# Kernel tuning notes

Measured on AMD Instinct MI355X. Metric: run time of the kernel, lower is better.

## Reference

```python
import jax, jax.numpy as jnp
import numpy as np

N = 50000
E = 800000
IN_DIM = 128
HID = 32
OUT_DIM = 64
HEADS = 4
NEG_SLOPE = 0.2  # DGL GATConv default leaky_relu slope


def setup_inputs() -> dict:
    key = jax.random.key(0)
    ks = jax.random.split(key, 16)
    h = jax.random.normal(ks[0], (N, IN_DIM), dtype=jnp.float32)
    src = jax.random.randint(ks[1], (E,), 0, N, dtype=jnp.int32)
    dst = jax.random.randint(ks[2], (E,), 0, N, dtype=jnp.int32)
    s = 0.05
    # layer 1: in 128 -> heads*32 = 128
    W1 = jax.random.normal(ks[3], (IN_DIM, HEADS * HID), dtype=jnp.float32) * s
    al1 = jax.random.normal(ks[4], (HEADS, HID), dtype=jnp.float32) * s
    ar1 = jax.random.normal(ks[5], (HEADS, HID), dtype=jnp.float32) * s
    # layer 2: in 128 -> heads*32 = 128
    W2 = jax.random.normal(ks[6], (HEADS * HID, HEADS * HID), dtype=jnp.float32) * s
    al2 = jax.random.normal(ks[7], (HEADS, HID), dtype=jnp.float32) * s
    ar2 = jax.random.normal(ks[8], (HEADS, HID), dtype=jnp.float32) * s
    # last layer: in 128 -> heads*64 = 256 (needs residual projection)
    W3 = jax.random.normal(ks[9], (HEADS * HID, HEADS * OUT_DIM), dtype=jnp.float32) * s
    al3 = jax.random.normal(ks[10], (HEADS, OUT_DIM), dtype=jnp.float32) * s
    ar3 = jax.random.normal(ks[11], (HEADS, OUT_DIM), dtype=jnp.float32) * s
    resW3 = jax.random.normal(ks[12], (HEADS * HID, HEADS * OUT_DIM), dtype=jnp.float32) * s
    return {"h": h, "W1": W1, "al1": al1, "ar1": ar1, "W2": W2, "al2": al2,
            "ar2": ar2, "W3": W3, "al3": al3, "ar3": ar3, "resW3": resW3,
            "src": src, "dst": dst}


def gat_layer(h, src, dst, W, al, ar, heads, out_feats, res_W=None, act=None):
    n = h.shape[0]
    feat = (h @ W).reshape(n, heads, out_feats)          # [N,H,D]
    el = jnp.einsum('nhd,hd->nh', feat, al)               # [N,H]
    er = jnp.einsum('nhd,hd->nh', feat, ar)               # [N,H]
    e = jax.nn.leaky_relu(el[src] + er[dst], NEG_SLOPE)   # [E,H]
    m = jax.ops.segment_max(e, dst, num_segments=n)       # per-dst max, [N,H]
    ex = jnp.exp(e - m[dst])
    denom = jax.ops.segment_sum(ex, dst, num_segments=n)  # [N,H]
    alpha = ex / denom[dst]                               # edge softmax, [E,H]
    msg = feat[src] * alpha[:, :, None]                   # [E,H,D]
    rst = jax.ops.segment_sum(msg, dst, num_segments=n)   # [N,H,D]
    res = (h @ res_W) if res_W is not None else h
    rst = rst + res.reshape(n, heads, out_feats)
    if act is not None:
        rst = act(rst)
    return rst


def reference(h, W1, al1, ar1, W2, al2, ar2, W3, al3, ar3, resW3, src, dst):
    n = h.shape[0]
    x = gat_layer(h, src, dst, W1, al1, ar1, HEADS, HID, act=jax.nn.relu)
    x = x.reshape(n, -1)
    # feat_drop=0.3 on layer 2 omitted (eval/deterministic mode)
    x = gat_layer(x, src, dst, W2, al2, ar2, HEADS, HID, act=jax.nn.relu)
    x = x.reshape(n, -1)
    x = gat_layer(x, src, dst, W3, al3, ar3, HEADS, OUT_DIM, res_W=resW3)
    return x.mean(axis=1)  # mean over heads -> [N, OUT_DIM]
```

## Files before the change

kernel.cpp:

```cpp
#include <hip/hip_runtime.h>
#include <hip/hip_bf16.h>
#include <math.h>


#define NEG_SLOPE 0.2f

typedef __attribute__((ext_vector_type(8))) __bf16 bf16x8;
typedef __attribute__((ext_vector_type(4))) float f32x4;

__device__ __forceinline__ float leaky(float x) { return fmaxf(x, NEG_SLOPE * x); }
__device__ __forceinline__ ushort f2bf(float f) {
    unsigned u = __float_as_uint(f);
    return (ushort)((u + 0x7fffu + ((u >> 16) & 1u)) >> 16);
}
__device__ __forceinline__ float bf2f(ushort b) { return __uint_as_float(((unsigned)b) << 16); }
__device__ __forceinline__ float lo16f(unsigned v) { return __uint_as_float(v << 16); }
__device__ __forceinline__ float hi16f(unsigned v) { return __uint_as_float(v & 0xffff0000u); }


__global__ void hist_kernel(const int* __restrict__ dst, int* __restrict__ deg, int E) {
    int i = blockIdx.x * blockDim.x + threadIdx.x;
    if (i < E) atomicAdd(&deg[dst[i]], 1);
}

__global__ void block_scan_kernel(const int* __restrict__ deg, int* __restrict__ loc,
                                  int* __restrict__ bsum, int n) {
    __shared__ int sm[1024];
    const int tid = threadIdx.x;
    const int i = blockIdx.x * 1024 + tid;
    int v = (i < n) ? deg[i] : 0;
    sm[tid] = v;
    __syncthreads();
    for (int off = 1; off < 1024; off <<= 1) {
        int t = (tid >= off) ? sm[tid - off] : 0;
        __syncthreads();
        sm[tid] += t;
        __syncthreads();
    }
    if (i < n) loc[i] = sm[tid] - v;
    if (tid == 1023) bsum[blockIdx.x] = sm[1023];
}

__global__ void scan_bsum_kernel(int* __restrict__ bsum, int nb, int* __restrict__ total_out) {
    const int lane = threadIdx.x;
    int v = (lane < nb) ? bsum[lane] : 0;
    int orig = v;
    for (int off = 1; off < 64; off <<= 1) {
        int t = __shfl_up(v, off);
        if (lane >= off) v += t;
    }
    if (lane < nb) bsum[lane] = v - orig;
    if (lane == 63) *total_out = v;
}

__global__ void apply_scan_kernel(const int* __restrict__ loc, const int* __restrict__ bsum,
                                  int* __restrict__ row_ptr, int* __restrict__ cursor, int n) {
    int i = blockIdx.x * blockDim.x + threadIdx.x;
    if (i < n) {
        int v = loc[i] + bsum[i >> 10];
        row_ptr[i] = v;
        cursor[i]  = v;
    }
}

__global__ void scatter_kernel(const int* __restrict__ src, const int* __restrict__ dst,
                               int* __restrict__ cursor, int* __restrict__ ssrc, int E) {
    int i = blockIdx.x * blockDim.x + threadIdx.x;
    if (i < E) {
        int s = src[i];
        int pos = atomicAdd(&cursor[dst[i]], 1);
        ssrc[pos] = s;
    }
}


__global__ void cast_split_kernel(const float* __restrict__ in, ushort* __restrict__ hi,
                                  ushort* __restrict__ lo, int n4) {
    int i = blockIdx.x * blockDim.x + threadIdx.x;
    if (i >= n4) return;
    float4 v = ((const float4*)in)[i];
    ushort4 h, l;
    h.x = f2bf(v.x); l.x = f2bf(v.x - bf2f(h.x));
    h.y = f2bf(v.y); l.y = f2bf(v.y - bf2f(h.y));
    h.z = f2bf(v.z); l.z = f2bf(v.z - bf2f(h.z));
    h.w = f2bf(v.w); l.w = f2bf(v.w - bf2f(h.w));
    ((ushort4*)hi)[i] = h;
    ((ushort4*)lo)[i] = l;
}

__global__ void castT_kernel(const float* __restrict__ in, ushort* __restrict__ hi, int Ncols) {
    int i = blockIdx.x * blockDim.x + threadIdx.x;
    if (i >= 128 * Ncols) return;
    int c = i >> 7, k = i & 127;
    float v = in[k * Ncols + c];
    int kd = k ^ ((c & 7) << 3);
    hi[c * 128 + kd] = f2bf(v);
}

__global__ void fold_resW_kernel(const float* __restrict__ rW3, ushort* __restrict__ hi) {
    int i = blockIdx.x * blockDim.x + threadIdx.x;
    if (i >= 64 * 128) return;
    int c = i >> 7, k = i & 127;
    const float* row = rW3 + (size_t)k * 256;
    float v = 0.25f * ((row[c] + row[64 + c]) + (row[128 + c] + row[192 + c]));
    int kd = k ^ ((c & 7) << 3);
    hi[c * 128 + kd] = f2bf(v);
}


__global__ void __launch_bounds__(256)
gemm_kernel(const ushort* __restrict__ Ah, const ushort* __restrict__ Bth,
            ushort* __restrict__ Cb, float* __restrict__ Cf,
            const float* __restrict__ alv, const float* __restrict__ arv,
            float* __restrict__ el, float* __restrict__ er,
            int M, int Ncols, int dshift) {
    __shared__ ushort Ws[64 * 128];
    const int tid = threadIdx.x;
    const int wv = tid >> 6;
    const int lane = tid & 63;
    const int l15 = lane & 15;
    const int g = lane >> 4;
    const int bm = blockIdx.x * 128 + wv * 32;
    const int bn = blockIdx.y * 64;

    {
        const uint4* gh = (const uint4*)(Bth + (size_t)bn * 128);
        uint4* sh = (uint4*)Ws;
#pragma unroll
        for (int it = 0; it < 4; ++it) {
            sh[it * 256 + tid] = gh[it * 256 + tid];
        }
    }
    __syncthreads();

    const int m0 = bm + l15;
    const int m1 = bm + 16 + l15;
    const int mc0 = (m0 < M) ? m0 : (M - 1);
    const int mc1 = (m1 < M) ? m1 : (M - 1);
    bf16x8 xh[2][4];
#pragma unroll
    for (int kk = 0; kk < 4; ++kk) {
        xh[0][kk] = *(const bf16x8*)(Ah + (size_t)mc0 * 128 + kk * 32 + g * 8);
        xh[1][kk] = *(const bf16x8*)(Ah + (size_t)mc1 * 128 + kk * 32 + g * 8);
    }

    f32x4 acc[2][4] = {};
    const int swz = (l15 & 7) << 4;
#pragma unroll
    for (int n = 0; n < 4; ++n) {
        const int colb = (n * 16 + l15) * 256;
#pragma unroll
        for (int kk = 0; kk < 4; ++kk) {
            const int boff = colb + ((kk * 64 + g * 16) ^ swz);
            bf16x8 wh = *(const bf16x8*)((const char*)Ws + boff);
            acc[0][n] = __builtin_amdgcn_mfma_f32_16x16x32_bf16(wh, xh[0][kk], acc[0][n], 0, 0, 0);
            acc[1][n] = __builtin_amdgcn_mfma_f32_16x16x32_bf16(wh, xh[1][kk], acc[1][n], 0, 0, 0);
        }
    }

#pragma unroll
    for (int mf = 0; mf < 2; ++mf) {
        const int m = (mf == 0) ? m0 : m1;
        const bool valid = (m < M);
        if (valid) {
            size_t ro = (size_t)m * Ncols;
#pragma unroll
            for (int n = 0; n < 4; ++n) {
                int col = bn + n * 16 + g * 4;
                if (Cb) {
                    ushort4 o;
                    o.x = f2bf(acc[mf][n][0]); o.y = f2bf(acc[mf][n][1]);
                    o.z = f2bf(acc[mf][n][2]); o.w = f2bf(acc[mf][n][3]);
                    *(ushort4*)&Cb[ro + col] = o;
                }
                if (Cf) {
                    *(float4*)&Cf[ro + col] = make_float4(acc[mf][n][0], acc[mf][n][1],
                                                          acc[mf][n][2], acc[mf][n][3]);
                }
            }
        }
        if (alv) {
            float e0 = 0.f, e1 = 0.f, r0 = 0.f, r1 = 0.f;
#pragma unroll
            for (int n = 0; n < 4; ++n) {
#pragma unroll
                for (int r = 0; r < 4; ++r) {
                    int col = n * 16 + g * 4 + r;
                    float c = acc[mf][n][r];
                    float av = alv[bn + col];
                    float bv = arv[bn + col];
                    if ((col >> dshift) == 0) { e0 += c * av; r0 += c * bv; }
                    else                      { e1 += c * av; r1 += c * bv; }
                }
            }
            e0 += __shfl_xor(e0, 16); e0 += __shfl_xor(e0, 32);
            e1 += __shfl_xor(e1, 16); e1 += __shfl_xor(e1, 32);
            r0 += __shfl_xor(r0, 16); r0 += __shfl_xor(r0, 32);
            r1 += __shfl_xor(r1, 16); r1 += __shfl_xor(r1, 32);
            if (valid && g == 0) {
                int h0 = bn >> dshift;
                el[m * 4 + h0] = e0;
                er[m * 4 + h0] = r0;
                if (dshift == 5) {
                    el[m * 4 + h0 + 1] = e1;
                    er[m * 4 + h0 + 1] = r1;
                }
            }
        }
    }
}


__global__ void __launch_bounds__(256)
aggregate12_kernel(const ushort* __restrict__ featb, const float* __restrict__ el,
                   const float* __restrict__ er, const int* __restrict__ row_ptr,
                   const int* __restrict__ ssrc, ushort* __restrict__ xbh,
                   ushort* __restrict__ xbl, int n) {
    const int wid = threadIdx.x >> 6;
    const int lane = threadIdx.x & 63;
    const int node = blockIdx.x * 4 + wid;
    if (node >= n) return;
    const int beg = row_ptr[node];
    const int end = row_ptr[node + 1];
    const int hh = lane >> 4;
    const float erh = er[node * 4 + hh];

    float ssum = 0.f, a0 = 0.f, a1 = 0.f;
    int p = beg;
    for (; p + 8 <= end; p += 8) {
        int s[8];
        float e[8];
        unsigned v[8];
#pragma unroll
        for (int j = 0; j < 8; ++j) s[j] = __builtin_amdgcn_readfirstlane(ssrc[p + j]);
#pragma unroll
        for (int j = 0; j < 8; ++j) v[j] = *(const unsigned*)&featb[(size_t)s[j] * 128 + lane * 2];
#pragma unroll
        for (int j = 0; j < 8; ++j) e[j] = el[s[j] * 4 + hh];
#pragma unroll
        for (int j = 0; j < 8; ++j) {
            float w0 = __expf(leaky(e[j] + erh));
            ssum += w0;
            a0 += w0 * lo16f(v[j]);
            a1 += w0 * hi16f(v[j]);
        }
    }
    for (; p < end; ++p) {
        int s = __builtin_amdgcn_readfirstlane(ssrc[p]);
        float w0 = __expf(leaky(el[s * 4 + hh] + erh));
        unsigned v = *(const unsigned*)&featb[(size_t)s * 128 + lane * 2];
        ssum += w0;
        a0 += w0 * lo16f(v);
        a1 += w0 * hi16f(v);
    }
    float inv = (end > beg) ? 1.f / ssum : 0.f;
    size_t o = (size_t)node * 128 + lane * 2;
    unsigned rh = *(const unsigned*)&xbh[o];
    unsigned rl = *(const unsigned*)&xbl[o];
    float r0 = fmaxf(a0 * inv + lo16f(rh) + lo16f(rl), 0.f);
    float r1 = fmaxf(a1 * inv + hi16f(rh) + hi16f(rl), 0.f);
    ushort h0 = f2bf(r0), h1 = f2bf(r1);
    ushort l0 = f2bf(r0 - bf2f(h0)), l1 = f2bf(r1 - bf2f(h1));
    *(unsigned*)&xbh[o] = (unsigned)h0 | ((unsigned)h1 << 16);
    *(unsigned*)&xbl[o] = (unsigned)l0 | ((unsigned)l1 << 16);
}


__global__ void __launch_bounds__(256)
aggregate3_kernel(const ushort* __restrict__ featb, const float* __restrict__ el,
                  const float* __restrict__ er, const int* __restrict__ row_ptr,
                  const int* __restrict__ ssrc, const float* __restrict__ resmean,
                  float* __restrict__ out, int n) {
    const int wid = threadIdx.x >> 6;
    const int lane = threadIdx.x & 63;
    const int node = blockIdx.x * 4 + wid;
    if (node >= n) return;
    const int beg = row_ptr[node];
    const int end = row_ptr[node + 1];
    const int hh = lane >> 4;
    const int dd = (lane & 15) * 4;
    const int off = hh * 64 + dd;
    const float erh = er[node * 4 + hh];

    float c0 = 0.f, c1 = 0.f, c2 = 0.f, c3 = 0.f, ssum = 0.f;
    int p = beg;
    for (; p + 8 <= end; p += 8) {
        int s[8];
        float e[8];
        uint2 v[8];
#pragma unroll
        for (int j = 0; j < 8; ++j) s[j] = __builtin_amdgcn_readfirstlane(ssrc[p + j]);
#pragma unroll
        for (int j = 0; j < 8; ++j) v[j] = *(const uint2*)&featb[(size_t)s[j] * 256 + off];
#pragma unroll
        for (int j = 0; j < 8; ++j) e[j] = el[s[j] * 4 + hh];
#pragma unroll
        for (int j = 0; j < 8; ++j) {
            float w0 = __expf(leaky(e[j] + erh));
            ssum += w0;
            c0 += w0 * lo16f(v[j].x);
            c1 += w0 * hi16f(v[j].x);
            c2 += w0 * lo16f(v[j].y);
            c3 += w0 * hi16f(v[j].y);
        }
    }
    for (; p < end; ++p) {
        int s = __builtin_amdgcn_readfirstlane(ssrc[p]);
        float w0 = __expf(leaky(el[s * 4 + hh] + erh));
        uint2 v = *(const uint2*)&featb[(size_t)s * 256 + off];
        ssum += w0;
        c0 += w0 * lo16f(v.x);
        c1 += w0 * hi16f(v.x);
        c2 += w0 * lo16f(v.y);
        c3 += w0 * hi16f(v.y);
    }
    float inv = (end > beg) ? 1.f / ssum : 0.f;
    float r0 = c0 * inv, r1 = c1 * inv, r2 = c2 * inv, r3 = c3 * inv;
    r0 += __shfl_xor(r0, 16); r0 += __shfl_xor(r0, 32);
    r1 += __shfl_xor(r1, 16); r1 += __shfl_xor(r1, 32);
    r2 += __shfl_xor(r2, 16); r2 += __shfl_xor(r2, 32);
    r3 += __shfl_xor(r3, 16); r3 += __shfl_xor(r3, 32);
    if (hh == 0) {
        float4 rm = *(const float4*)&resmean[(size_t)node * 64 + dd];
        *(float4*)&out[(size_t)node * 64 + dd] =
            make_float4(0.25f * r0 + rm.x, 0.25f * r1 + rm.y,
                        0.25f * r2 + rm.z, 0.25f * r3 + rm.w);
    }
}


extern "C" void kernel_launch(void* const* d_in, const int* in_sizes, int n_in,
                              void* d_out, int out_size, void* d_ws, size_t ws_size,
                              hipStream_t stream) {
    const float* h   = (const float*)d_in[0];
    const float* W1  = (const float*)d_in[1];
    const float* al1 = (const float*)d_in[2];
    const float* ar1 = (const float*)d_in[3];
    const float* W2  = (const float*)d_in[4];
    const float* al2 = (const float*)d_in[5];
    const float* ar2 = (const float*)d_in[6];
    const float* W3  = (const float*)d_in[7];
    const float* al3 = (const float*)d_in[8];
    const float* ar3 = (const float*)d_in[9];
    const float* rW3 = (const float*)d_in[10];
    const int* src   = (const int*)d_in[11];
    const int* dstv  = (const int*)d_in[12];
    const int N = in_sizes[0] / 128;
    const int E = in_sizes[11];
    float* out = (float*)d_out;

    char* p = (char*)d_ws;
    auto alloc = [&](size_t bytes) -> char* {
        char* q = p;
        p += (bytes + 255) & ~(size_t)255;
        return q;
    };
    int*    row_ptr = (int*)alloc((size_t)(N + 1) * 4);
    int*    cursor  = (int*)alloc((size_t)N * 4);
    int*    loc     = (int*)alloc((size_t)N * 4);
    int*    bsum    = (int*)alloc(64 * 4);
    int*    ssrc    = (int*)alloc((size_t)E * 4);
    float*  el      = (float*)alloc((size_t)N * 16);
    float*  er      = (float*)alloc((size_t)N * 16);
    ushort* featb   = (ushort*)alloc((size_t)N * 256 * 2);
    ushort* xbh     = (ushort*)alloc((size_t)N * 128 * 2);
    ushort* xbl     = (ushort*)alloc((size_t)N * 128 * 2);
    ushort* W1th = (ushort*)alloc(128 * 128 * 2);
    ushort* W2th = (ushort*)alloc(128 * 128 * 2);
    ushort* W3th = (ushort*)alloc(256 * 128 * 2);
    ushort* rWmh = (ushort*)alloc(64 * 128 * 2);
    float*  resmean = (float*)alloc((size_t)N * 64 * 4);

    hipMemsetAsync(cursor, 0, (size_t)N * 4, stream);
    hist_kernel<<<(E + 255) / 256, 256, 0, stream>>>(dstv, cursor, E);
    int nb = (N + 1023) / 1024;
    block_scan_kernel<<<nb, 1024, 0, stream>>>(cursor, loc, bsum, N);
    scan_bsum_kernel<<<1, 64, 0, stream>>>(bsum, nb, row_ptr + N);
    apply_scan_kernel<<<(N + 255) / 256, 256, 0, stream>>>(loc, bsum, row_ptr, cursor, N);
    scatter_kernel<<<(E + 255) / 256, 256, 0, stream>>>(src, dstv, cursor, ssrc, E);

    cast_split_kernel<<<(N * 128 / 4 + 255) / 256, 256, 0, stream>>>(h, xbh, xbl, N * 128 / 4);
    castT_kernel<<<(128 * 128 + 255) / 256, 256, 0, stream>>>(W1, W1th, 128);
    castT_kernel<<<(128 * 128 + 255) / 256, 256, 0, stream>>>(W2, W2th, 128);
    castT_kernel<<<(128 * 256 + 255) / 256, 256, 0, stream>>>(W3, W3th, 256);
    fold_resW_kernel<<<(64 * 128 + 255) / 256, 256, 0, stream>>>(rW3, rWmh);

    const int gx = (N + 127) / 128;
    dim3 g1(gx, 2);
    dim3 g3(gx, 4);
    dim3 gr(gx, 1);
    int agg_grid = (N + 3) / 4;

    gemm_kernel<<<g1, 256, 0, stream>>>(xbh, W1th, featb, nullptr,
                                        al1, ar1, el, er, N, 128, 5);
    aggregate12_kernel<<<agg_grid, 256, 0, stream>>>(featb, el, er, row_ptr, ssrc, xbh, xbl, N);

    gemm_kernel<<<g1, 256, 0, stream>>>(xbh, W2th, featb, nullptr,
                                        al2, ar2, el, er, N, 128, 5);
    aggregate12_kernel<<<agg_grid, 256, 0, stream>>>(featb, el, er, row_ptr, ssrc, xbh, xbl, N);

    gemm_kernel<<<g3, 256, 0, stream>>>(xbh, W3th, featb, nullptr,
                                        al3, ar3, el, er, N, 256, 6);
    gemm_kernel<<<gr, 256, 0, stream>>>(xbh, rWmh, nullptr, resmean,
                                        nullptr, nullptr, nullptr, nullptr, N, 64, 6);
    aggregate3_kernel<<<agg_grid, 256, 0, stream>>>(featb, el, er, row_ptr, ssrc, resmean, out, N);
}
```

Measured before the change: 418.3 us.

## Fuse prep casts into one kernel, merge residual GEMM into layer-3 GEMM

Five small cast/transpose kernels become one prep kernel, which now writes only the bf16 high part of h. Layer 1's residual is read as fp32 straight from h in the aggregate kernel, so the lo buffer is no longer written there. The separate residual-projection GEMM is folded into the layer-3 GEMM: blocks with blockIdx.y==0 also load the folded residual weights into LDS and compute a second accumulator. This saves launches and a second read of xbh, but makes y==0 blocks do more work and doubles dynamic LDS for all blocks of that launch, which may lower occupancy.

After: 401.7 us. 1.04x faster.

```diff
diff --git a/kernel.cpp b/kernel.cpp
--- a/kernel.cpp
+++ b/kernel.cpp
@@ -74,47 +74,55 @@
 }
 
 
-__global__ void cast_split_kernel(const float* __restrict__ in, ushort* __restrict__ hi,
-                                  ushort* __restrict__ lo, int n4) {
+__global__ void prep_kernel(const float* __restrict__ h, ushort* __restrict__ xbh,
+                            const float* __restrict__ W1, ushort* __restrict__ W1th,
+                            const float* __restrict__ W2, ushort* __restrict__ W2th,
+                            const float* __restrict__ W3, ushort* __restrict__ W3th,
+                            const float* __restrict__ rW3, ushort* __restrict__ rWmh,
+                            int nh4) {
     int i = blockIdx.x * blockDim.x + threadIdx.x;
-    if (i >= n4) return;
-    float4 v = ((const float4*)in)[i];
-    ushort4 h, l;
-    h.x = f2bf(v.x); l.x = f2bf(v.x - bf2f(h.x));
-    h.y = f2bf(v.y); l.y = f2bf(v.y - bf2f(h.y));
-    h.z = f2bf(v.z); l.z = f2bf(v.z - bf2f(h.z));
-    h.w = f2bf(v.w); l.w = f2bf(v.w - bf2f(h.w));
-    ((ushort4*)hi)[i] = h;
-    ((ushort4*)lo)[i] = l;
-}
-
-__global__ void castT_kernel(const float* __restrict__ in, ushort* __restrict__ hi, int Ncols) {
-    int i = blockIdx.x * blockDim.x + threadIdx.x;
-    if (i >= 128 * Ncols) return;
-    int c = i >> 7, k = i & 127;
-    float v = in[k * Ncols + c];
-    int kd = k ^ ((c & 7) << 3);
-    hi[c * 128 + kd] = f2bf(v);
-}
-
-__global__ void fold_resW_kernel(const float* __restrict__ rW3, ushort* __restrict__ hi) {
-    int i = blockIdx.x * blockDim.x + threadIdx.x;
-    if (i >= 64 * 128) return;
-    int c = i >> 7, k = i & 127;
-    const float* row = rW3 + (size_t)k * 256;
-    float v = 0.25f * ((row[c] + row[64 + c]) + (row[128 + c] + row[192 + c]));
-    int kd = k ^ ((c & 7) << 3);
-    hi[c * 128 + kd] = f2bf(v);
+    if (i < nh4) {
+        float4 v = ((const float4*)h)[i];
+        ushort4 o;
+        o.x = f2bf(v.x); o.y = f2bf(v.y); o.z = f2bf(v.z); o.w = f2bf(v.w);
+        ((ushort4*)xbh)[i] = o;
+        return;
+    }
+    int j = i - nh4;
+    if (j < 16384) {
+        int c = j >> 7, k = j & 127;
+        int kd = k ^ ((c & 7) << 3);
+        W1th[c * 128 + kd] = f2bf(W1[k * 128 + c]);
+    } else if (j < 32768) {
+        j -= 16384;
+        int c = j >> 7, k = j & 127;
+        int kd = k ^ ((c & 7) << 3);
+        W2th[c * 128 + kd] = f2bf(W2[k * 128 + c]);
+    } else if (j < 65536) {
+        j -= 32768;
+        int c = j >> 7, k = j & 127;
+        int kd = k ^ ((c & 7) << 3);
+        W3th[c * 128 + kd] = f2bf(W3[k * 256 + c]);
+    } else if (j < 73728) {
+        j -= 65536;
+        int c = j >> 7, k = j & 127;
+        const float* row = rW3 + (size_t)k * 256;
+        float v = 0.25f * ((row[c] + row[64 + c]) + (row[128 + c] + row[192 + c]));
+        int kd = k ^ ((c & 7) << 3);
+        rWmh[c * 128 + kd] = f2bf(v);
+    }
 }
 
 
 __global__ void __launch_bounds__(256)
 gemm_kernel(const ushort* __restrict__ Ah, const ushort* __restrict__ Bth,
-            ushort* __restrict__ Cb, float* __restrict__ Cf,
+            const ushort* __restrict__ B2th,
+            ushort* __restrict__ Cb, float* __restrict__ C2f,
             const float* __restrict__ alv, const float* __restrict__ arv,
             float* __restrict__ el, float* __restrict__ er,
             int M, int Ncols, int dshift) {
-    __shared__ ushort Ws[64 * 128];
+    extern __shared__ ushort Ws[];
+    ushort* Ws2 = Ws + 64 * 128;
     const int tid = threadIdx.x;
     const int wv = tid >> 6;
     const int lane = tid & 63;
@@ -122,13 +130,18 @@
     const int g = lane >> 4;
     const int bm = blockIdx.x * 128 + wv * 32;
     const int bn = blockIdx.y * 64;
+    const bool do2 = (B2th != nullptr) && (blockIdx.y == 0);
 
     {
         const uint4* gh = (const uint4*)(Bth + (size_t)bn * 128);
         uint4* sh = (uint4*)Ws;
 #pragma unroll
-        for (int it = 0; it < 4; ++it) {
-            sh[it * 256 + tid] = gh[it * 256 + tid];
+        for (int it = 0; it < 4; ++it) sh[it * 256 + tid] = gh[it * 256 + tid];
+        if (do2) {
+            const uint4* g2 = (const uint4*)B2th;
+            uint4* s2 = (uint4*)Ws2;
+#pragma unroll
+            for (int it = 0; it < 4; ++it) s2[it * 256 + tid] = g2[it * 256 + tid];
         }
     }
     __syncthreads();
@@ -145,6 +158,7 @@
     }
 
     f32x4 acc[2][4] = {};
+    f32x4 acc2[2][4] = {};
     const int swz = (l15 & 7) << 4;
 #pragma unroll
     for (int n = 0; n < 4; ++n) {
@@ -155,6 +169,11 @@
             bf16x8 wh = *(const bf16x8*)((const char*)Ws + boff);
             acc[0][n] = __builtin_amdgcn_mfma_f32_16x16x32_bf16(wh, xh[0][kk], acc[0][n], 0, 0, 0);
             acc[1][n] = __builtin_amdgcn_mfma_f32_16x16x32_bf16(wh, xh[1][kk], acc[1][n], 0, 0, 0);
+            if (do2) {
+                bf16x8 w2 = *(const bf16x8*)((const char*)Ws2 + boff);
+                acc2[0][n] = __builtin_amdgcn_mfma_f32_16x16x32_bf16(w2, xh[0][kk], acc2[0][n], 0, 0, 0);
+                acc2[1][n] = __builtin_amdgcn_mfma_f32_16x16x32_bf16(w2, xh[1][kk], acc2[1][n], 0, 0, 0);
+            }
         }
     }
 
@@ -167,15 +186,14 @@
 #pragma unroll
             for (int n = 0; n < 4; ++n) {
                 int col = bn + n * 16 + g * 4;
-                if (Cb) {
-                    ushort4 o;
-                    o.x = f2bf(acc[mf][n][0]); o.y = f2bf(acc[mf][n][1]);
-                    o.z = f2bf(acc[mf][n][2]); o.w = f2bf(acc[mf][n][3]);
-                    *(ushort4*)&Cb[ro + col] = o;
-                }
-                if (Cf) {
-                    *(float4*)&Cf[ro + col] = make_float4(acc[mf][n][0], acc[mf][n][1],
-                                                          acc[mf][n][2], acc[mf][n][3]);
+                ushort4 o;
+                o.x = f2bf(acc[mf][n][0]); o.y = f2bf(acc[mf][n][1]);
+                o.z = f2bf(acc[mf][n][2]); o.w = f2bf(acc[mf][n][3]);
+                *(ushort4*)&Cb[ro + col] = o;
+                if (do2) {
+                    *(float4*)&C2f[(size_t)m * 64 + n * 16 + g * 4] =
+                        make_float4(acc2[mf][n][0], acc2[mf][n][1],
+                                    acc2[mf][n][2], acc2[mf][n][3]);
                 }
             }
         }
@@ -214,8 +232,9 @@
 __global__ void __launch_bounds__(256)
 aggregate12_kernel(const ushort* __restrict__ featb, const float* __restrict__ el,
                    const float* __restrict__ er, const int* __restrict__ row_ptr,
-                   const int* __restrict__ ssrc, ushort* __restrict__ xbh,
-                   ushort* __restrict__ xbl, int n) {
+                   const int* __restrict__ ssrc, const float* __restrict__ resf,
+                   const ushort* __restrict__ rxh, const ushort* __restrict__ rxl,
+                   ushort* __restrict__ xbh, ushort* __restrict__ xbl, int n) {
     const int wid = threadIdx.x >> 6;
     const int lane = threadIdx.x & 63;
     const int node = blockIdx.x * 4 + wid;
@@ -255,10 +274,18 @@
     }
     float inv = (end > beg) ? 1.f / ssum : 0.f;
     size_t o = (size_t)node * 128 + lane * 2;
-    unsigned rh = *(const unsigned*)&xbh[o];
-    unsigned rl = *(const unsigned*)&xbl[o];
-    float r0 = fmaxf(a0 * inv + lo16f(rh) + lo16f(rl), 0.f);
-    float r1 = fmaxf(a1 * inv + hi16f(rh) + hi16f(rl), 0.f);
+    float rb0, rb1;
+    if (resf) {
+        float2 f = *(const float2*)&resf[o];
+        rb0 = f.x; rb1 = f.y;
+    } else {
+        unsigned rh = *(const unsigned*)&rxh[o];
+        unsigned rl = *(const unsigned*)&rxl[o];
+        rb0 = lo16f(rh) + lo16f(rl);
+        rb1 = hi16f(rh) + hi16f(rl);
+    }
+    float r0 = fmaxf(a0 * inv + rb0, 0.f);
+    float r1 = fmaxf(a1 * inv + rb1, 0.f);
     ushort h0 = f2bf(r0), h1 = f2bf(r1);
     ushort l0 = f2bf(r0 - bf2f(h0)), l1 = f2bf(r1 - bf2f(h1));
     *(unsigned*)&xbh[o] = (unsigned)h0 | ((unsigned)h1 << 16);
@@ -379,29 +406,28 @@
     apply_scan_kernel<<<(N + 255) / 256, 256, 0, stream>>>(loc, bsum, row_ptr, cursor, N);
     scatter_kernel<<<(E + 255) / 256, 256, 0, stream>>>(src, dstv, cursor, ssrc, E);
 
-    cast_split_kernel<<<(N * 128 / 4 + 255) / 256, 256, 0, stream>>>(h, xbh, xbl, N * 128 / 4);
-    castT_kernel<<<(128 * 128 + 255) / 256, 256, 0, stream>>>(W1, W1th, 128);
-    castT_kernel<<<(128 * 128 + 255) / 256, 256, 0, stream>>>(W2, W2th, 128);
-    castT_kernel<<<(128 * 256 + 255) / 256, 256, 0, stream>>>(W3, W3th, 256);
-    fold_resW_kernel<<<(64 * 128 + 255) / 256, 256, 0, stream>>>(rW3, rWmh);
+    const int nh4 = N * 32;
+    prep_kernel<<<(nh4 + 73728 + 255) / 256, 256, 0, stream>>>(
+        h, xbh, W1, W1th, W2, W2th, W3, W3th, rW3, rWmh, nh4);
 
     const int gx = (N + 127) / 128;
     dim3 g1(gx, 2);
     dim3 g3(gx, 4);
-    dim3 gr(gx, 1);
     int agg_grid = (N + 3) / 4;
-
-    gemm_kernel<<<g1, 256, 0, stream>>>(xbh, W1th, featb, nullptr,
-                                        al1, ar1, el, er, N, 128, 5);
-    aggregate12_kernel<<<agg_grid, 256, 0, stream>>>(featb, el, er, row_ptr, ssrc, xbh, xbl, N);
-
-    gemm_kernel<<<g1, 256, 0, stream>>>(xbh, W2th, featb, nullptr,
-                                        al2, ar2, el, er, N, 128, 5);
-    aggregate12_kernel<<<agg_grid, 256, 0, stream>>>(featb, el, er, row_ptr, ssrc, xbh, xbl, N);
-
-    gemm_kernel<<<g3, 256, 0, stream>>>(xbh, W3th, featb, nullptr,
-                                        al3, ar3, el, er, N, 256, 6);
-    gemm_kernel<<<gr, 256, 0, stream>>>(xbh, rWmh, nullptr, resmean,
-                                        nullptr, nullptr, nullptr, nullptr, N, 64, 6);
+    const size_t lds1 = 64 * 128 * sizeof(ushort);
+    const size_t lds2 = 2 * 64 * 128 * sizeof(ushort);
+
+    gemm_kernel<<<g1, 256, lds1, stream>>>(xbh, W1th, nullptr, featb, nullptr,
+                                           al1, ar1, el, er, N, 128, 5);
+    aggregate12_kernel<<<agg_grid, 256, 0, stream>>>(featb, el, er, row_ptr, ssrc,
+                                                     h, nullptr, nullptr, xbh, xbl, N);
+
+    gemm_kernel<<<g1, 256, lds1, stream>>>(xbh, W2th, nullptr, featb, nullptr,
+                                           al2, ar2, el, er, N, 128, 5);
+    aggregate12_kernel<<<agg_grid, 256, 0, stream>>>(featb, el, er, row_ptr, ssrc,
+                                                     nullptr, xbh, xbl, xbh, xbl, N);
+
+    gemm_kernel<<<g3, 256, lds2, stream>>>(xbh, W3th, rWmh, featb, resmean,
+                                           al3, ar3, el, er, N, 256, 6);
     aggregate3_kernel<<<agg_grid, 256, 0, stream>>>(featb, el, er, row_ptr, ssrc, resmean, out, N);
 }
```
